# Optimization experiments

Measured on AMD Instinct MI355X. Metric: run time of the kernel, lower is better.

Reference implementation:

```python
import jax, jax.numpy as jnp
import numpy as np

H = 1024      # hidden_size
I = 2048      # expert intermediate_size (SwiGLU)
E = 8         # num_local_experts
B, S = 2, 4096
EPS = 1e-5
INIT = 0.02


def setup_inputs() -> dict:
    key = jax.random.key(0)
    ks = jax.random.split(key, 9)
    return {
        "hidden_states": jax.random.normal(ks[0], (B, S, H), jnp.float32),
        "ln_w": jnp.ones((H,), jnp.float32),
        "ln_b": jnp.zeros((H,), jnp.float32),
        "router_w": jax.random.normal(ks[1], (H, E), jnp.float32) * INIT,
        "gate_w": jax.random.normal(ks[2], (E, H, I), jnp.float32) * INIT,
        "up_w": jax.random.normal(ks[3], (E, H, I), jnp.float32) * INIT,
        "down_w": jax.random.normal(ks[4], (E, I, H), jnp.float32) * INIT,
        "sh_gate": jax.random.normal(ks[5], (H, I), jnp.float32) * INIT,
        "sh_up": jax.random.normal(ks[6], (H, I), jnp.float32) * INIT,
        "sh_down": jax.random.normal(ks[7], (I, H), jnp.float32) * INIT,
    }


def _layernorm(x, w, b):
    mu = jnp.mean(x, axis=-1, keepdims=True)
    var = jnp.mean(jnp.square(x - mu), axis=-1, keepdims=True)
    return (x - mu) * jax.lax.rsqrt(var + EPS) * w + b


def reference(hidden_states, ln_w, ln_b, router_w, gate_w, up_w, down_w,
              sh_gate, sh_up, sh_down):
    b, s, h = hidden_states.shape
    normed = _layernorm(hidden_states, ln_w, ln_b)
    xf = normed.reshape(-1, h)                       # [T, H]

    # Router: top-1 expert per token, sigmoid gating (Llama-4 style)
    logits = xf @ router_w                           # [T, E]
    top_idx = jnp.argmax(logits, axis=-1)            # [T]
    top_score = jax.nn.sigmoid(jnp.max(logits, axis=-1))  # [T]

    # Routed experts: scan over experts, mask+scale tokens assigned to each.
    def body(acc, ew):
        g, u, d, e = ew
        w = jnp.where(top_idx == e, top_score, 0.0)[:, None]  # [T, 1]
        xe = xf * w                                            # gate score applied to input
        hmid = jax.nn.silu(xe @ g) * (xe @ u)                  # [T, I]
        return acc + hmid @ d, None

    routed, _ = jax.lax.scan(
        body, jnp.zeros_like(xf), (gate_w, up_w, down_w, jnp.arange(E)))

    # Shared expert (dense SwiGLU) applied to all tokens
    shared = (jax.nn.silu(xf @ sh_gate) * (xf @ sh_up)) @ sh_down  # [T, H]

    moe_out = (routed + shared).reshape(b, s, h)
    return hidden_states + moe_out
```

## Files before the change

### kernel.cpp

```cpp
#include <hip/hip_runtime.h>

typedef unsigned short ushort_t;
typedef unsigned int uint_t;

#define T_TOK 8192
#define HDIM 1024
#define IDIM 2048
#define NEXP 8
#define RPAD_MAX 10240
#define TOTROWS (RPAD_MAX + T_TOK)

using f32x4 = __attribute__((ext_vector_type(4))) float;
using s16x8 = __attribute__((ext_vector_type(8))) short;

#define SBAR() do { asm volatile("" ::: "memory"); __builtin_amdgcn_s_barrier(); asm volatile("" ::: "memory"); } while (0)
#define VMW(n) asm volatile("s_waitcnt vmcnt(" #n ")" ::: "memory")
#define LGKM(n) do { asm volatile("s_waitcnt lgkmcnt(" #n ")" ::: "memory"); __builtin_amdgcn_sched_barrier(0); } while (0)
#define SCHB() __builtin_amdgcn_sched_barrier(0)

__device__ __forceinline__ float b2f(ushort_t h) {
    return __uint_as_float(((uint_t)h) << 16);
}
__device__ __forceinline__ ushort_t f2bf(float f) {
    uint_t u = __float_as_uint(f);
    uint_t r = (u + 0x7FFFu + ((u >> 16) & 1u)) >> 16;
    return (ushort_t)r;
}
__device__ __forceinline__ void gload16(const void* g, void* l) {
    __builtin_amdgcn_global_load_lds(
        (const __attribute__((address_space(1))) void*)g,
        (__attribute__((address_space(3))) void*)l, 16, 0, 0);
}
__device__ __forceinline__ void sbmap(int bid, int SBC, int NSB, int& rt, int& ct) {
    int x = bid & 7, j = bid >> 3;
    int r = j >> 5, pos = j & 31;
    int sb = r * 8 + x;
    int rem = NSB - r * 8;
    if (rem < 8) {
        int share = 8 / rem;
        int cap = 32 / share;
        sb = r * 8 + x / share;
        pos = (x % share) * cap + (pos % cap);
    }
    int sbr = sb / SBC, sbc = sb % SBC;
    rt = sbr * 4 + (pos >> 3);
    ct = sbc * 8 + (pos & 7);
}

__global__ void tcvt64(const float* __restrict__ gw, const float* __restrict__ shg,
                       const float* __restrict__ uw, const float* __restrict__ shu,
                       const float* __restrict__ dw, const float* __restrict__ shd,
                       ushort_t* __restrict__ gwt, ushort_t* __restrict__ uwt,
                       ushort_t* __restrict__ dwt) {
    __shared__ float tile[64][65];
    int z = blockIdx.z;
    const float* src;
    ushort_t* dst;
    int R, C, bx = blockIdx.x, by = blockIdx.y;
    if (z < 18) {
        int zz = z % 9;
        R = HDIM; C = IDIM;
        if (z < 9) { src = zz < 8 ? gw + (size_t)zz * HDIM * IDIM : shg; dst = gwt + (size_t)zz * IDIM * HDIM; }
        else       { src = zz < 8 ? uw + (size_t)zz * HDIM * IDIM : shu; dst = uwt + (size_t)zz * IDIM * HDIM; }
    } else {
        int zz = z - 18;
        R = IDIM; C = HDIM;
        src = zz < 8 ? dw + (size_t)zz * IDIM * HDIM : shd;
        dst = dwt + (size_t)zz * HDIM * IDIM;
        int t = bx; bx = by; by = t;
    }
    int c0 = bx * 64, r0 = by * 64;
    int tx = threadIdx.x, ty = threadIdx.y;
#pragma unroll
    for (int i = 0; i < 16; ++i)
        tile[ty + i * 4][tx] = src[(size_t)(r0 + ty + i * 4) * C + c0 + tx];
    __syncthreads();
    int tid = ty * 64 + tx;
    int rr = (tid & 15) * 4, cc0 = tid >> 4;
#pragma unroll
    for (int it = 0; it < 4; ++it) {
        int c = cc0 + it * 16;
        ushort4 v;
        v.x = f2bf(tile[rr + 0][c]);
        v.y = f2bf(tile[rr + 1][c]);
        v.z = f2bf(tile[rr + 2][c]);
        v.w = f2bf(tile[rr + 3][c]);
        *(ushort4*)&dst[(size_t)(c0 + c) * R + r0 + rr] = v;
    }
}

__global__ void ln_router(const float* __restrict__ x, const float* __restrict__ lnw,
                          const float* __restrict__ lnb, const float* __restrict__ rw,
                          ushort_t* __restrict__ normed, int* __restrict__ top_idx,
                          float* __restrict__ top_score, int* __restrict__ cnt) {
    int t = blockIdx.x, tid = threadIdx.x;
    const float* xr = x + (size_t)t * HDIM;
    float v[4];
    float s = 0.f, ss = 0.f;
#pragma unroll
    for (int i = 0; i < 4; i++) {
        v[i] = xr[tid + i * 256];
        s += v[i];
        ss += v[i] * v[i];
    }
#pragma unroll
    for (int o = 32; o; o >>= 1) {
        s += __shfl_down(s, o);
        ss += __shfl_down(ss, o);
    }
    __shared__ float rs_[4], rss_[4], stats[2];
    int wid = tid >> 6, lane = tid & 63;
    if (!lane) { rs_[wid] = s; rss_[wid] = ss; }
    __syncthreads();
    if (!tid) {
        float S = rs_[0] + rs_[1] + rs_[2] + rs_[3];
        float SS = rss_[0] + rss_[1] + rss_[2] + rss_[3];
        float mu = S * (1.f / HDIM);
        float var = SS * (1.f / HDIM) - mu * mu;
        stats[0] = mu;
        stats[1] = rsqrtf(var + 1e-5f);
    }
    __syncthreads();
    float mu = stats[0], rsg = stats[1];
    float lg[8] = {0, 0, 0, 0, 0, 0, 0, 0};
#pragma unroll
    for (int i = 0; i < 4; i++) {
        int h = tid + i * 256;
        float xn = (v[i] - mu) * rsg * lnw[h] + lnb[h];
        normed[(size_t)t * HDIM + h] = f2bf(xn);
        const float* rwh = rw + (size_t)h * NEXP;
#pragma unroll
        for (int e = 0; e < 8; e++) lg[e] += xn * rwh[e];
    }
#pragma unroll
    for (int o = 32; o; o >>= 1)
#pragma unroll
        for (int e = 0; e < 8; e++) lg[e] += __shfl_down(lg[e], o);
    __shared__ float lred[4][8];
    if (!lane)
#pragma unroll
        for (int e = 0; e < 8; e++) lred[wid][e] = lg[e];
    __syncthreads();
    if (!tid) {
        float best = -1e30f;
        int bi = 0;
#pragma unroll
        for (int e = 0; e < 8; e++) {
            float L = lred[0][e] + lred[1][e] + lred[2][e] + lred[3][e];
            if (L > best) { best = L; bi = e; }
        }
        top_idx[t] = bi;
        top_score[t] = 1.f / (1.f + __expf(-best));
        atomicAdd(&cnt[bi], 1);
    }
}

__global__ void scan_k(const int* __restrict__ cnt, int* __restrict__ pad_off,
                       int* __restrict__ fill) {
    if (threadIdx.x == 0) {
        int o = 0;
        for (int e = 0; e < NEXP; e++) {
            pad_off[e] = o;
            o += (cnt[e] + 255) & ~255;
        }
        pad_off[NEXP] = o;
    }
    if (threadIdx.x < NEXP) fill[threadIdx.x] = 0;
}

__global__ void scatter_k(const ushort_t* __restrict__ normed, const int* __restrict__ top_idx,
                          const float* __restrict__ top_score, const int* __restrict__ pad_off,
                          int* __restrict__ fill, int* __restrict__ order,
                          ushort_t* __restrict__ xs) {
    int t = blockIdx.x, tid = threadIdx.x;
    __shared__ int spos;
    if (!tid) {
        int e = top_idx[t];
        int p = pad_off[e] + atomicAdd(&fill[e], 1);
        order[p] = t;
        spos = p;
    }
    __syncthreads();
    int pos = spos;
    float sc = top_score[t];
    const ushort4* src = (const ushort4*)(normed + (size_t)t * HDIM);
    ushort4* dst = (ushort4*)(xs + (size_t)pos * HDIM);
    ushort4 a = src[tid];
    a.x = f2bf(b2f(a.x) * sc);
    a.y = f2bf(b2f(a.y) * sc);
    a.z = f2bf(b2f(a.z) * sc);
    a.w = f2bf(b2f(a.w) * sc);
    dst[tid] = a;
}

__global__ __launch_bounds__(512, 2) void gemm1_k(
    const ushort_t* __restrict__ X, const ushort_t* __restrict__ Wg,
    const ushort_t* __restrict__ Wu, const int* __restrict__ pad_off,
    ushort_t* __restrict__ hmid) {
    __shared__ __align__(16) ushort_t lds[2 * 32768];
    const int CT = IDIM / 128;
    const int NH = HDIM / 64;
    int rt, ct;
    sbmap(blockIdx.x, CT / 8, (TOTROWS / 256 / 4) * (CT / 8), rt, ct);
    int row0 = rt * 256, col0 = ct * 128;
    int e;
    if (row0 >= RPAD_MAX) e = 8;
    else {
        if (row0 >= pad_off[NEXP]) return;
        e = 0;
        while (e < 7 && row0 >= pad_off[e + 1]) ++e;
    }
    const ushort_t* wgp = Wg + (size_t)e * IDIM * HDIM;
    const ushort_t* wup = Wu + (size_t)e * IDIM * HDIM;

    const int tid = threadIdx.x, l = tid & 63, w = tid >> 6;
    const int wm = w >> 2, wn = w & 3;
    const int lr = l & 15, lg4 = l >> 4;

    const ushort_t* sA[4];
#pragma unroll
    for (int j = 0; j < 4; ++j) {
        int gi = tid + j * 512, row = gi >> 3, kg = (gi & 7) ^ (row & 7);
        sA[j] = X + (size_t)(row0 + row) * HDIM + kg * 8;
    }
    const ushort_t *sBg[2], *sBu[2];
#pragma unroll
    for (int j = 0; j < 2; ++j) {
        int gi = tid + j * 512, row = gi >> 3, kg = (gi & 7) ^ (row & 7);
        sBg[j] = wgp + (size_t)(col0 + row) * HDIM + kg * 8;
        sBu[j] = wup + (size_t)(col0 + row) * HDIM + kg * 8;
    }
    const int sl0 = (lg4 ^ (lr & 7)) * 8, sl1 = ((4 + lg4) ^ (lr & 7)) * 8;
    const int aob = (wm * 128 + lr) * 64;
    const int bob = (wn * 32 + lr) * 64;

    f32x4 accg[8][2] = {};
    f32x4 accu[8][2] = {};

#define G1_STAGE(h) do { int ko = (h) * 64; int hb_ = ((h) & 1) * 32768;       \
        gload16(sA[0] + ko, &lds[hb_ + tid * 8]);                              \
        gload16(sA[1] + ko, &lds[hb_ + 4096 + tid * 8]);                       \
        gload16(sA[2] + ko, &lds[hb_ + 8192 + tid * 8]);                       \
        gload16(sA[3] + ko, &lds[hb_ + 12288 + tid * 8]);                      \
        gload16(sBg[0] + ko, &lds[hb_ + 16384 + tid * 8]);                     \
        gload16(sBg[1] + ko, &lds[hb_ + 20480 + tid * 8]);                     \
        gload16(sBu[0] + ko, &lds[hb_ + 24576 + tid * 8]);                     \
        gload16(sBu[1] + ko, &lds[hb_ + 28672 + tid * 8]); } while (0)

#define G1_PH(h, DOSTAGE) do {                                                 \
        const int hb = ((h) & 1) * 32768;                                      \
        s16x8 a0[8], a1[8], b0[4], b1[4];                                      \
        _Pragma("unroll")                                                      \
        for (int m = 0; m < 8; ++m) a0[m] = *(const s16x8*)&lds[hb + aob + m * 1024 + sl0]; \
        _Pragma("unroll")                                                      \
        for (int n = 0; n < 2; ++n) {                                          \
            b0[n] = *(const s16x8*)&lds[hb + 16384 + bob + n * 1024 + sl0];    \
            b0[2 + n] = *(const s16x8*)&lds[hb + 24576 + bob + n * 1024 + sl0]; \
        }                                                                      \
        SCHB();                                                                \
        _Pragma("unroll")                                                      \
        for (int m = 0; m < 8; ++m) a1[m] = *(const s16x8*)&lds[hb + aob + m * 1024 + sl1]; \
        _Pragma("unroll")                                                      \
        for (int n = 0; n < 2; ++n) {                                          \
            b1[n] = *(const s16x8*)&lds[hb + 16384 + bob + n * 1024 + sl1];    \
            b1[2 + n] = *(const s16x8*)&lds[hb + 24576 + bob + n * 1024 + sl1]; \
        }                                                                      \
        SCHB();                                                                \
        if (DOSTAGE) G1_STAGE((h) + 1);                                        \
        LGKM(12);                                                              \
        __builtin_amdgcn_s_setprio(1);                                         \
        _Pragma("unroll")                                                      \
        for (int m = 0; m < 8; ++m) {                                          \
            accg[m][0] = __builtin_amdgcn_mfma_f32_16x16x32_bf16(a0[m], b0[0], accg[m][0], 0, 0, 0); \
            accg[m][1] = __builtin_amdgcn_mfma_f32_16x16x32_bf16(a0[m], b0[1], accg[m][1], 0, 0, 0); \
            accu[m][0] = __builtin_amdgcn_mfma_f32_16x16x32_bf16(a0[m], b0[2], accu[m][0], 0, 0, 0); \
            accu[m][1] = __builtin_amdgcn_mfma_f32_16x16x32_bf16(a0[m], b0[3], accu[m][1], 0, 0, 0); \
        }                                                                      \
        __builtin_amdgcn_s_setprio(0);                                         \
        LGKM(0);                                                               \
        __builtin_amdgcn_s_setprio(1);                                         \
        _Pragma("unroll")                                                      \
        for (int m = 0; m < 8; ++m) {                                          \
            accg[m][0] = __builtin_amdgcn_mfma_f32_16x16x32_bf16(a1[m], b1[0], accg[m][0], 0, 0, 0); \
            accg[m][1] = __builtin_amdgcn_mfma_f32_16x16x32_bf16(a1[m], b1[1], accg[m][1], 0, 0, 0); \
            accu[m][0] = __builtin_amdgcn_mfma_f32_16x16x32_bf16(a1[m], b1[2], accu[m][0], 0, 0, 0); \
            accu[m][1] = __builtin_amdgcn_mfma_f32_16x16x32_bf16(a1[m], b1[3], accu[m][1], 0, 0, 0); \
        }                                                                      \
        __builtin_amdgcn_s_setprio(0);                                         \
        VMW(0);                                                                \
        SBAR();                                                                \
    } while (0)

    G1_STAGE(0);
    VMW(0);
    SBAR();
    for (int h = 0; h < NH - 1; ++h) G1_PH(h, 1);
    G1_PH(NH - 1, 0);

#pragma unroll
    for (int mf = 0; mf < 8; ++mf) {
        int row = row0 + wm * 128 + mf * 16 + lg4 * 4;
#pragma unroll
        for (int nf = 0; nf < 2; ++nf) {
            int col = col0 + wn * 32 + nf * 16 + lr;
#pragma unroll
            for (int rr = 0; rr < 4; ++rr) {
                float g = accg[mf][nf][rr], u = accu[mf][nf][rr];
                float val = g / (1.f + __expf(-g)) * u;
                hmid[(size_t)(row + rr) * IDIM + col] = f2bf(val);
            }
        }
    }
#undef G1_STAGE
#undef G1_PH
}

template <int SHARED>
__global__ __launch_bounds__(512, 2) void gemm2_k(
    const ushort_t* __restrict__ Hm, const ushort_t* __restrict__ Wd,
    const int* __restrict__ pad_off, const int* __restrict__ order,
    const float* __restrict__ hs, float* __restrict__ out, int RT) {
    __shared__ __align__(16) ushort_t lds[2 * 32768];
    const int CT = 4;
    const int NH = IDIM / 64;
    int nwg = RT * CT;
    int bid = blockIdx.x;
    int q = nwg >> 3, r = nwg & 7;
    int xcd = bid & 7, idx = bid >> 3;
    int wg = (xcd < r ? xcd * (q + 1) : r * (q + 1) + (xcd - r) * q) + idx;
    int rt = wg >> 2, ct = wg & 3;
    int row0 = rt * 256, col0 = ct * 256;
    const ushort_t* wdp;
    if (SHARED) {
        wdp = Wd + (size_t)8 * HDIM * IDIM;
    } else {
        if (row0 >= pad_off[NEXP]) return;
        int e = 0;
        while (e < 7 && row0 >= pad_off[e + 1]) ++e;
        wdp = Wd + (size_t)e * HDIM * IDIM;
    }
    const int tid = threadIdx.x, l = tid & 63, w = tid >> 6;
    const int wm = w >> 2, wn = w & 3;
    const int lr = l & 15, lg4 = l >> 4;

    const ushort_t* sA[4];
    const ushort_t* sB[4];
#pragma unroll
    for (int j = 0; j < 4; ++j) {
        int gi = tid + j * 512, row = gi >> 3, kg = (gi & 7) ^ (row & 7);
        sA[j] = Hm + (size_t)(row0 + row) * IDIM + kg * 8;
        sB[j] = wdp + (size_t)(col0 + row) * IDIM + kg * 8;
    }
    const int sl0 = (lg4 ^ (lr & 7)) * 8, sl1 = ((4 + lg4) ^ (lr & 7)) * 8;
    const int aob = (wm * 128 + lr) * 64;
    const int bob = (wn * 64 + lr) * 64;

    f32x4 acc[8][4] = {};

#define G2_STAGE(h) do { int ko = (h) * 64; int hb_ = ((h) & 1) * 32768;       \
        gload16(sA[0] + ko, &lds[hb_ + tid * 8]);                              \
        gload16(sA[1] + ko, &lds[hb_ + 4096 + tid * 8]);                       \
        gload16(sA[2] + ko, &lds[hb_ + 8192 + tid * 8]);                       \
        gload16(sA[3] + ko, &lds[hb_ + 12288 + tid * 8]);                      \
        gload16(sB[0] + ko, &lds[hb_ + 16384 + tid * 8]);                      \
        gload16(sB[1] + ko, &lds[hb_ + 20480 + tid * 8]);                      \
        gload16(sB[2] + ko, &lds[hb_ + 24576 + tid * 8]);                      \
        gload16(sB[3] + ko, &lds[hb_ + 28672 + tid * 8]); } while (0)

#define G2_PH(h, DOSTAGE) do {                                                 \
        const int hb = ((h) & 1) * 32768;                                      \
        s16x8 a0[8], a1[8], b0[4], b1[4];                                      \
        _Pragma("unroll")                                                      \
        for (int m = 0; m < 8; ++m) a0[m] = *(const s16x8*)&lds[hb + aob + m * 1024 + sl0]; \
        _Pragma("unroll")                                                      \
        for (int n = 0; n < 4; ++n) b0[n] = *(const s16x8*)&lds[hb + 16384 + bob + n * 1024 + sl0]; \
        SCHB();                                                                \
        _Pragma("unroll")                                                      \
        for (int m = 0; m < 8; ++m) a1[m] = *(const s16x8*)&lds[hb + aob + m * 1024 + sl1]; \
        _Pragma("unroll")                                                      \
        for (int n = 0; n < 4; ++n) b1[n] = *(const s16x8*)&lds[hb + 16384 + bob + n * 1024 + sl1]; \
        SCHB();                                                                \
        if (DOSTAGE) G2_STAGE((h) + 1);                                        \
        LGKM(12);                                                              \
        __builtin_amdgcn_s_setprio(1);                                         \
        _Pragma("unroll")                                                      \
        for (int m = 0; m < 8; ++m)                                            \
            _Pragma("unroll")                                                  \
            for (int n = 0; n < 4; ++n)                                        \
                acc[m][n] = __builtin_amdgcn_mfma_f32_16x16x32_bf16(a0[m], b0[n], acc[m][n], 0, 0, 0); \
        __builtin_amdgcn_s_setprio(0);                                         \
        LGKM(0);                                                               \
        __builtin_amdgcn_s_setprio(1);                                         \
        _Pragma("unroll")                                                      \
        for (int m = 0; m < 8; ++m)                                            \
            _Pragma("unroll")                                                  \
            for (int n = 0; n < 4; ++n)                                        \
                acc[m][n] = __builtin_amdgcn_mfma_f32_16x16x32_bf16(a1[m], b1[n], acc[m][n], 0, 0, 0); \
        __builtin_amdgcn_s_setprio(0);                                         \
        VMW(0);                                                                \
        SBAR();                                                                \
    } while (0)

    G2_STAGE(0);
    VMW(0);
    SBAR();
    for (int h = 0; h < NH - 1; ++h) G2_PH(h, 1);
    G2_PH(NH - 1, 0);

#pragma unroll
    for (int mf = 0; mf < 8; ++mf) {
        int row = row0 + wm * 128 + mf * 16 + lg4 * 4;
#pragma unroll
        for (int rr = 0; rr < 4; ++rr) {
            int rw_ = row + rr;
            int tok;
            if (SHARED) tok = rw_;
            else { tok = order[rw_]; if (tok < 0) continue; }
            size_t ob = (size_t)tok * HDIM;
#pragma unroll
            for (int nf = 0; nf < 4; ++nf) {
                int col = col0 + wn * 64 + nf * 16 + lr;
                if (SHARED) out[ob + col] += hs[ob + col] + acc[mf][nf][rr];
                else        out[ob + col] = acc[mf][nf][rr];
            }
        }
    }
#undef G2_STAGE
#undef G2_PH
}

extern "C" void kernel_launch(void* const* d_in, const int* in_sizes, int n_in,
                              void* d_out, int out_size, void* d_ws, size_t ws_size,
                              hipStream_t stream) {
    const float* hs = (const float*)d_in[0];
    const float* lnw = (const float*)d_in[1];
    const float* lnb = (const float*)d_in[2];
    const float* rw = (const float*)d_in[3];
    const float* gw = (const float*)d_in[4];
    const float* uw = (const float*)d_in[5];
    const float* dw = (const float*)d_in[6];
    const float* shg = (const float*)d_in[7];
    const float* shu = (const float*)d_in[8];
    const float* shd = (const float*)d_in[9];
    float* out = (float*)d_out;

    char* p = (char*)d_ws;
    auto alloc = [&](size_t bytes) {
        void* r = (void*)p;
        p += (bytes + 255) & ~(size_t)255;
        return r;
    };
    ushort_t* xsbuf = (ushort_t*)alloc((size_t)TOTROWS * HDIM * 2);
    ushort_t* hmid = (ushort_t*)alloc((size_t)TOTROWS * IDIM * 2);
    ushort_t* gwt = (ushort_t*)alloc((size_t)9 * IDIM * HDIM * 2);
    ushort_t* uwt = (ushort_t*)alloc((size_t)9 * IDIM * HDIM * 2);
    ushort_t* dwt = (ushort_t*)alloc((size_t)9 * HDIM * IDIM * 2);
    int* cnt = (int*)alloc(NEXP * 4);
    int* pad_off = (int*)alloc((NEXP + 1) * 4);
    int* fill = (int*)alloc(NEXP * 4);
    int* top_idx = (int*)alloc(T_TOK * 4);
    float* top_sc = (float*)alloc(T_TOK * 4);
    int* order = (int*)alloc(RPAD_MAX * 4);

    ushort_t* normed = xsbuf + (size_t)RPAD_MAX * HDIM;

    hipMemsetAsync(cnt, 0, NEXP * 4, stream);
    hipMemsetAsync(order, 0xFF, RPAD_MAX * 4, stream);
    hipMemsetAsync(xsbuf, 0, (size_t)RPAD_MAX * HDIM * 2, stream);

    tcvt64<<<dim3(IDIM / 64, HDIM / 64, 27), dim3(64, 4), 0, stream>>>(
        gw, shg, uw, shu, dw, shd, gwt, uwt, dwt);

    ln_router<<<T_TOK, 256, 0, stream>>>(hs, lnw, lnb, rw, normed, top_idx, top_sc, cnt);
    scan_k<<<1, 64, 0, stream>>>(cnt, pad_off, fill);
    scatter_k<<<T_TOK, 256, 0, stream>>>(normed, top_idx, top_sc, pad_off, fill, order, xsbuf);

    {
        int RT = TOTROWS / 256, CT = IDIM / 128;
        gemm1_k<<<RT * CT, 512, 0, stream>>>(xsbuf, gwt, uwt, pad_off, hmid);
    }
    {
        int RT = RPAD_MAX / 256;
        gemm2_k<0><<<RT * 4, 512, 0, stream>>>(
            hmid, dwt, pad_off, order, hs, out, RT);
    }
    {
        int RT = T_TOK / 256;
        gemm2_k<1><<<RT * 4, 512, 0, stream>>>(
            hmid + (size_t)RPAD_MAX * IDIM, dwt, pad_off, order, hs, out, RT);
    }
}
```

Before: 562.8 us.

## Merge routed and shared down-projection GEMMs into one launch with separate add

The two gemm2 launches (routed experts, then shared expert) are fused into a single 288-workgroup grid covering both row segments, so the GPU can fill its compute units with both workloads at once instead of running two partially occupied launches back to back. The routed results go to a new scratch buffer, the shared results plus residual go straight to out, and a small elementwise add kernel combines them. This costs an extra 32MB fp32 write and read-modify-write pass, plus one more launch.

```diff
diff --git a/kernel.cpp b/kernel.cpp
--- a/kernel.cpp
+++ b/kernel.cpp
@@ -315,23 +315,20 @@
 #undef G1_PH
 }
 
-template <int SHARED>
-__global__ __launch_bounds__(512, 2) void gemm2_k(
+__global__ __launch_bounds__(512, 2) void gemm2f_k(
     const ushort_t* __restrict__ Hm, const ushort_t* __restrict__ Wd,
     const int* __restrict__ pad_off, const int* __restrict__ order,
-    const float* __restrict__ hs, float* __restrict__ out, int RT) {
+    const float* __restrict__ hs, float* __restrict__ out,
+    float* __restrict__ out2) {
     __shared__ __align__(16) ushort_t lds[2 * 32768];
-    const int CT = 4;
     const int NH = IDIM / 64;
-    int nwg = RT * CT;
     int bid = blockIdx.x;
-    int q = nwg >> 3, r = nwg & 7;
-    int xcd = bid & 7, idx = bid >> 3;
-    int wg = (xcd < r ? xcd * (q + 1) : r * (q + 1) + (xcd - r) * q) + idx;
+    int wg = (bid & 7) * 36 + (bid >> 3);
     int rt = wg >> 2, ct = wg & 3;
     int row0 = rt * 256, col0 = ct * 256;
+    int seg_shared = (row0 >= RPAD_MAX);
     const ushort_t* wdp;
-    if (SHARED) {
+    if (seg_shared) {
         wdp = Wd + (size_t)8 * HDIM * IDIM;
     } else {
         if (row0 >= pad_off[NEXP]) return;
@@ -413,20 +410,29 @@
 #pragma unroll
         for (int rr = 0; rr < 4; ++rr) {
             int rw_ = row + rr;
-            int tok;
-            if (SHARED) tok = rw_;
-            else { tok = order[rw_]; if (tok < 0) continue; }
-            size_t ob = (size_t)tok * HDIM;
 #pragma unroll
             for (int nf = 0; nf < 4; ++nf) {
                 int col = col0 + wn * 64 + nf * 16 + lr;
-                if (SHARED) out[ob + col] += hs[ob + col] + acc[mf][nf][rr];
-                else        out[ob + col] = acc[mf][nf][rr];
+                if (seg_shared) {
+                    size_t ob = (size_t)(rw_ - RPAD_MAX) * HDIM + col;
+                    out[ob] = hs[ob] + acc[mf][nf][rr];
+                } else {
+                    int tok = order[rw_];
+                    if (tok >= 0) out2[(size_t)tok * HDIM + col] = acc[mf][nf][rr];
+                }
             }
         }
     }
 #undef G2_STAGE
 #undef G2_PH
+}
+
+__global__ void add_k(float* __restrict__ out, const float* __restrict__ out2) {
+    size_t i = ((size_t)blockIdx.x * 256 + threadIdx.x) * 4;
+    float4 a = *(float4*)&out[i];
+    float4 b = *(const float4*)&out2[i];
+    a.x += b.x; a.y += b.y; a.z += b.z; a.w += b.w;
+    *(float4*)&out[i] = a;
 }
 
 extern "C" void kernel_launch(void* const* d_in, const int* in_sizes, int n_in,
@@ -455,6 +461,7 @@
     ushort_t* gwt = (ushort_t*)alloc((size_t)9 * IDIM * HDIM * 2);
     ushort_t* uwt = (ushort_t*)alloc((size_t)9 * IDIM * HDIM * 2);
     ushort_t* dwt = (ushort_t*)alloc((size_t)9 * HDIM * IDIM * 2);
+    float* out2 = (float*)alloc((size_t)T_TOK * HDIM * 4);
     int* cnt = (int*)alloc(NEXP * 4);
     int* pad_off = (int*)alloc((NEXP + 1) * 4);
     int* fill = (int*)alloc(NEXP * 4);
@@ -479,14 +486,6 @@
         int RT = TOTROWS / 256, CT = IDIM / 128;
         gemm1_k<<<RT * CT, 512, 0, stream>>>(xsbuf, gwt, uwt, pad_off, hmid);
     }
-    {
-        int RT = RPAD_MAX / 256;
-        gemm2_k<0><<<RT * 4, 512, 0, stream>>>(
-            hmid, dwt, pad_off, order, hs, out, RT);
-    }
-    {
-        int RT = T_TOK / 256;
-        gemm2_k<1><<<RT * 4, 512, 0, stream>>>(
-            hmid + (size_t)RPAD_MAX * IDIM, dwt, pad_off, order, hs, out, RT);
-    }
-}
+    gemm2f_k<<<288, 512, 0, stream>>>(hmid, dwt, pad_off, order, hs, out, out2);
+    add_k<<<(T_TOK * HDIM) / (256 * 4), 256, 0, stream>>>(out, out2);
+}
```

Result: slower. 626.0 us (+11.2%).

## Vectorize weight transpose and use one wave per token in LN/router and scatter

Applied to the files above, without the earlier changes.

The weight transpose-convert kernel now loads float4 and stores 16-byte bf16 vectors. LayerNorm/router and scatter kernels process one token per wavefront, four tokens per block, using xor shuffles instead of shared-memory reductions and block barriers. This targets wider memory transactions and fewer syncs in the preprocessing kernels, at the cost of possible LDS bank conflicts in the transpose's column reads.

```diff
diff --git a/kernel.cpp b/kernel.cpp
--- a/kernel.cpp
+++ b/kernel.cpp
@@ -47,11 +47,12 @@
     ct = sbc * 8 + (pos & 7);
 }
 
-__global__ void tcvt64(const float* __restrict__ gw, const float* __restrict__ shg,
-                       const float* __restrict__ uw, const float* __restrict__ shu,
-                       const float* __restrict__ dw, const float* __restrict__ shd,
-                       ushort_t* __restrict__ gwt, ushort_t* __restrict__ uwt,
-                       ushort_t* __restrict__ dwt) {
+__global__ __launch_bounds__(256) void tcvt64(
+    const float* __restrict__ gw, const float* __restrict__ shg,
+    const float* __restrict__ uw, const float* __restrict__ shu,
+    const float* __restrict__ dw, const float* __restrict__ shd,
+    ushort_t* __restrict__ gwt, ushort_t* __restrict__ uwt,
+    ushort_t* __restrict__ dwt) {
     __shared__ float tile[64][65];
     int z = blockIdx.z;
     const float* src;
@@ -70,85 +71,80 @@
         int t = bx; bx = by; by = t;
     }
     int c0 = bx * 64, r0 = by * 64;
-    int tx = threadIdx.x, ty = threadIdx.y;
-#pragma unroll
-    for (int i = 0; i < 16; ++i)
-        tile[ty + i * 4][tx] = src[(size_t)(r0 + ty + i * 4) * C + c0 + tx];
+    int t = threadIdx.x;
+    int rrow = t >> 4, cg = (t & 15) * 4;
+#pragma unroll
+    for (int i = 0; i < 4; ++i) {
+        int row = rrow + i * 16;
+        float4 v = *(const float4*)&src[(size_t)(r0 + row) * C + c0 + cg];
+        tile[row][cg] = v.x;
+        tile[row][cg + 1] = v.y;
+        tile[row][cg + 2] = v.z;
+        tile[row][cg + 3] = v.w;
+    }
     __syncthreads();
-    int tid = ty * 64 + tx;
-    int rr = (tid & 15) * 4, cc0 = tid >> 4;
-#pragma unroll
-    for (int it = 0; it < 4; ++it) {
-        int c = cc0 + it * 16;
-        ushort4 v;
-        v.x = f2bf(tile[rr + 0][c]);
-        v.y = f2bf(tile[rr + 1][c]);
-        v.z = f2bf(tile[rr + 2][c]);
-        v.w = f2bf(tile[rr + 3][c]);
-        *(ushort4*)&dst[(size_t)(c0 + c) * R + r0 + rr] = v;
-    }
-}
-
-__global__ void ln_router(const float* __restrict__ x, const float* __restrict__ lnw,
-                          const float* __restrict__ lnb, const float* __restrict__ rw,
-                          ushort_t* __restrict__ normed, int* __restrict__ top_idx,
-                          float* __restrict__ top_score, int* __restrict__ cnt) {
-    int t = blockIdx.x, tid = threadIdx.x;
-    const float* xr = x + (size_t)t * HDIM;
-    float v[4];
+    int cw = t >> 3, rg = (t & 7) * 8;
+#pragma unroll
+    for (int i = 0; i < 2; ++i) {
+        int c = cw + i * 32;
+        s16x8 o;
+#pragma unroll
+        for (int j = 0; j < 8; ++j) o[j] = (short)f2bf(tile[rg + j][c]);
+        *(s16x8*)&dst[(size_t)(c0 + c) * R + r0 + rg] = o;
+    }
+}
+
+__global__ __launch_bounds__(256) void ln_router(
+    const float* __restrict__ x, const float* __restrict__ lnw,
+    const float* __restrict__ lnb, const float* __restrict__ rw,
+    ushort_t* __restrict__ normed, int* __restrict__ top_idx,
+    float* __restrict__ top_score, int* __restrict__ cnt) {
+    int w = threadIdx.x >> 6, lane = threadIdx.x & 63;
+    int t = blockIdx.x * 4 + w;
+    const float4* xr = (const float4*)(x + (size_t)t * HDIM);
+    float4 v[4];
     float s = 0.f, ss = 0.f;
 #pragma unroll
-    for (int i = 0; i < 4; i++) {
-        v[i] = xr[tid + i * 256];
-        s += v[i];
-        ss += v[i] * v[i];
-    }
-#pragma unroll
-    for (int o = 32; o; o >>= 1) {
-        s += __shfl_down(s, o);
-        ss += __shfl_down(ss, o);
-    }
-    __shared__ float rs_[4], rss_[4], stats[2];
-    int wid = tid >> 6, lane = tid & 63;
-    if (!lane) { rs_[wid] = s; rss_[wid] = ss; }
-    __syncthreads();
-    if (!tid) {
-        float S = rs_[0] + rs_[1] + rs_[2] + rs_[3];
-        float SS = rss_[0] + rss_[1] + rss_[2] + rss_[3];
-        float mu = S * (1.f / HDIM);
-        float var = SS * (1.f / HDIM) - mu * mu;
-        stats[0] = mu;
-        stats[1] = rsqrtf(var + 1e-5f);
-    }
-    __syncthreads();
-    float mu = stats[0], rsg = stats[1];
+    for (int i = 0; i < 4; ++i) {
+        v[i] = xr[lane + i * 64];
+        s += v[i].x + v[i].y + v[i].z + v[i].w;
+        ss += v[i].x * v[i].x + v[i].y * v[i].y + v[i].z * v[i].z + v[i].w * v[i].w;
+    }
+#pragma unroll
+    for (int m = 32; m; m >>= 1) {
+        s += __shfl_xor(s, m);
+        ss += __shfl_xor(ss, m);
+    }
+    float mu = s * (1.f / HDIM);
+    float rsg = rsqrtf(ss * (1.f / HDIM) - mu * mu + 1e-5f);
     float lg[8] = {0, 0, 0, 0, 0, 0, 0, 0};
 #pragma unroll
-    for (int i = 0; i < 4; i++) {
-        int h = tid + i * 256;
-        float xn = (v[i] - mu) * rsg * lnw[h] + lnb[h];
-        normed[(size_t)t * HDIM + h] = f2bf(xn);
-        const float* rwh = rw + (size_t)h * NEXP;
-#pragma unroll
-        for (int e = 0; e < 8; e++) lg[e] += xn * rwh[e];
-    }
-#pragma unroll
-    for (int o = 32; o; o >>= 1)
-#pragma unroll
-        for (int e = 0; e < 8; e++) lg[e] += __shfl_down(lg[e], o);
-    __shared__ float lred[4][8];
-    if (!lane)
-#pragma unroll
-        for (int e = 0; e < 8; e++) lred[wid][e] = lg[e];
-    __syncthreads();
-    if (!tid) {
+    for (int i = 0; i < 4; ++i) {
+        int h0 = (lane + i * 64) * 4;
+        float4 lw = *(const float4*)&lnw[h0];
+        float4 lb = *(const float4*)&lnb[h0];
+        float xn0 = (v[i].x - mu) * rsg * lw.x + lb.x;
+        float xn1 = (v[i].y - mu) * rsg * lw.y + lb.y;
+        float xn2 = (v[i].z - mu) * rsg * lw.z + lb.z;
+        float xn3 = (v[i].w - mu) * rsg * lw.w + lb.w;
+        ushort4 o;
+        o.x = f2bf(xn0); o.y = f2bf(xn1); o.z = f2bf(xn2); o.w = f2bf(xn3);
+        *(ushort4*)&normed[(size_t)t * HDIM + h0] = o;
+        const float* rp = rw + (size_t)h0 * NEXP;
+#pragma unroll
+        for (int e = 0; e < 8; ++e)
+            lg[e] += xn0 * rp[e] + xn1 * rp[8 + e] + xn2 * rp[16 + e] + xn3 * rp[24 + e];
+    }
+#pragma unroll
+    for (int m = 32; m; m >>= 1)
+#pragma unroll
+        for (int e = 0; e < 8; ++e) lg[e] += __shfl_xor(lg[e], m);
+    if (!lane) {
         float best = -1e30f;
         int bi = 0;
 #pragma unroll
-        for (int e = 0; e < 8; e++) {
-            float L = lred[0][e] + lred[1][e] + lred[2][e] + lred[3][e];
-            if (L > best) { best = L; bi = e; }
-        }
+        for (int e = 0; e < 8; ++e)
+            if (lg[e] > best) { best = lg[e]; bi = e; }
         top_idx[t] = bi;
         top_score[t] = 1.f / (1.f + __expf(-best));
         atomicAdd(&cnt[bi], 1);
@@ -168,29 +164,30 @@
     if (threadIdx.x < NEXP) fill[threadIdx.x] = 0;
 }
 
-__global__ void scatter_k(const ushort_t* __restrict__ normed, const int* __restrict__ top_idx,
-                          const float* __restrict__ top_score, const int* __restrict__ pad_off,
-                          int* __restrict__ fill, int* __restrict__ order,
-                          ushort_t* __restrict__ xs) {
-    int t = blockIdx.x, tid = threadIdx.x;
-    __shared__ int spos;
-    if (!tid) {
+__global__ __launch_bounds__(256) void scatter_k(
+    const ushort_t* __restrict__ normed, const int* __restrict__ top_idx,
+    const float* __restrict__ top_score, const int* __restrict__ pad_off,
+    int* __restrict__ fill, int* __restrict__ order, ushort_t* __restrict__ xs) {
+    int w = threadIdx.x >> 6, lane = threadIdx.x & 63;
+    int t = blockIdx.x * 4 + w;
+    int p = 0;
+    if (!lane) {
         int e = top_idx[t];
-        int p = pad_off[e] + atomicAdd(&fill[e], 1);
+        p = pad_off[e] + atomicAdd(&fill[e], 1);
         order[p] = t;
-        spos = p;
-    }
-    __syncthreads();
-    int pos = spos;
+    }
+    p = __shfl(p, 0);
     float sc = top_score[t];
-    const ushort4* src = (const ushort4*)(normed + (size_t)t * HDIM);
-    ushort4* dst = (ushort4*)(xs + (size_t)pos * HDIM);
-    ushort4 a = src[tid];
-    a.x = f2bf(b2f(a.x) * sc);
-    a.y = f2bf(b2f(a.y) * sc);
-    a.z = f2bf(b2f(a.z) * sc);
-    a.w = f2bf(b2f(a.w) * sc);
-    dst[tid] = a;
+    const s16x8* src = (const s16x8*)(normed + (size_t)t * HDIM);
+    s16x8* dst = (s16x8*)(xs + (size_t)p * HDIM);
+#pragma unroll
+    for (int j = 0; j < 2; ++j) {
+        s16x8 a = src[lane + j * 64];
+        s16x8 o;
+#pragma unroll
+        for (int k = 0; k < 8; ++k) o[k] = (short)f2bf(b2f((ushort_t)a[k]) * sc);
+        dst[lane + j * 64] = o;
+    }
 }
 
 __global__ __launch_bounds__(512, 2) void gemm1_k(
@@ -468,12 +465,12 @@
     hipMemsetAsync(order, 0xFF, RPAD_MAX * 4, stream);
     hipMemsetAsync(xsbuf, 0, (size_t)RPAD_MAX * HDIM * 2, stream);
 
-    tcvt64<<<dim3(IDIM / 64, HDIM / 64, 27), dim3(64, 4), 0, stream>>>(
+    tcvt64<<<dim3(IDIM / 64, HDIM / 64, 27), 256, 0, stream>>>(
         gw, shg, uw, shu, dw, shd, gwt, uwt, dwt);
 
-    ln_router<<<T_TOK, 256, 0, stream>>>(hs, lnw, lnb, rw, normed, top_idx, top_sc, cnt);
+    ln_router<<<T_TOK / 4, 256, 0, stream>>>(hs, lnw, lnb, rw, normed, top_idx, top_sc, cnt);
     scan_k<<<1, 64, 0, stream>>>(cnt, pad_off, fill);
-    scatter_k<<<T_TOK, 256, 0, stream>>>(normed, top_idx, top_sc, pad_off, fill, order, xsbuf);
+    scatter_k<<<T_TOK / 4, 256, 0, stream>>>(normed, top_idx, top_sc, pad_off, fill, order, xsbuf);
 
     {
         int RT = TOTROWS / 256, CT = IDIM / 128;
```

Result: slower. 578.3 us (+2.8%).
